# Optimization experiments

Measured on AMD Instinct MI355X. Metric: run time of the kernel, lower is better.

The kernel has to match this reference:

```python
import jax, jax.numpy as jnp
import numpy as np

IN_DIM = 5000
OUT_DIM = 30
K = 50
BATCH = 16384


def setup_inputs() -> dict:
    key = jax.random.key(0)
    ks = jax.random.split(key, 8)
    return {
        "x": jax.random.normal(ks[0], (BATCH, IN_DIM), dtype=jnp.float32),
        "logits": jax.random.normal(ks[1], (IN_DIM,), dtype=jnp.float32),
        "W1": jax.random.normal(ks[2], (IN_DIM, 32), dtype=jnp.float32) * (1.0 / np.sqrt(IN_DIM)),
        "b1": jax.random.normal(ks[3], (32,), dtype=jnp.float32) * 0.01,
        "W2": jax.random.normal(ks[4], (32, 16), dtype=jnp.float32) * (1.0 / np.sqrt(32)),
        "b2": jax.random.normal(ks[5], (16,), dtype=jnp.float32) * 0.01,
        "W3": jax.random.normal(ks[6], (16, OUT_DIM), dtype=jnp.float32) * (1.0 / np.sqrt(16)),
        "b3": jax.random.normal(ks[7], (OUT_DIM,), dtype=jnp.float32) * 0.01,
        "epoch": 10,
        "total_epochs": 100,
    }


def reference(x, logits, W1, b1, W2, b2, W3, b3, epoch, total_epochs):
    # Eval path (training=False): top-k one-hot mask over the learned logits.
    # indices of top-k logits -> k-hot mask of shape [in_dim]
    _, idx = jax.lax.top_k(logits, K)                 # [K]
    mask = jnp.zeros_like(logits).at[idx].set(1.0)    # [in_dim], k-hot
    xm = mask * x                                      # [B, in_dim] gated input
    h = jax.nn.relu(xm @ W1 + b1)                      # [B, 32]
    h = jax.nn.relu(h @ W2 + b2)                       # [B, 16]
    out = h @ W3 + b3                                  # [B, out_dim]
    return out, mask
```

## Files before the change

### kernel.cpp

```cpp
#include <hip/hip_runtime.h>
#include <hip/hip_bf16.h>

#define N_IN 5000
#define K_SEL 50
#define B_ROWS 16384
#define OUT_D 30

__global__ __launch_bounds__(1024) void topk_mask_kernel(
    const float* __restrict__ logits,
    float* __restrict__ mask,
    int* __restrict__ idx_out)
{
    __shared__ unsigned int s_cnt[34];
    __shared__ int s_tick, s_sel;

    const int tid  = threadIdx.x;
    const int lane = tid & 63;

    if (tid < 34) s_cnt[tid] = 0u;
    if (tid == 40) { s_tick = 0; }
    if (tid == 41) { s_sel = 0; }

    unsigned int key[5];
#pragma unroll
    for (int j = 0; j < 5; j++) {
        int i = tid + j * 1024;
        if (i < N_IN) {
            unsigned int b = __float_as_uint(logits[i]);
            key[j] = (b & 0x80000000u) ? ~b : (b | 0x80000000u);
            mask[i] = 0.0f;
        } else {
            key[j] = 0u;
        }
    }
    __syncthreads();

    unsigned int lo = 0u, hi = 0xFFFFFFFFu;
    for (int iter = 0; iter < 32; iter++) {
        if (lo >= hi) break;
        unsigned int mid = lo + ((hi - lo) >> 1) + 1u;
        unsigned int c = 0;
#pragma unroll
        for (int j = 0; j < 5; j++) c += (key[j] >= mid) ? 1u : 0u;
#pragma unroll
        for (int off = 32; off > 0; off >>= 1) c += __shfl_down(c, off, 64);
        if (lane == 0) atomicAdd(&s_cnt[iter], c);
        __syncthreads();
        unsigned int cnt = s_cnt[iter];
        if (cnt >= (unsigned)K_SEL) lo = mid; else hi = mid - 1u;
    }
    const unsigned int KT = lo;

    {
        unsigned int c = 0;
#pragma unroll
        for (int j = 0; j < 5; j++) c += (key[j] > KT) ? 1u : 0u;
#pragma unroll
        for (int off = 32; off > 0; off >>= 1) c += __shfl_down(c, off, 64);
        if (lane == 0) atomicAdd(&s_cnt[33], c);
    }
    __syncthreads();
    const int rem = K_SEL - (int)s_cnt[33];

#pragma unroll
    for (int j = 0; j < 5; j++) {
        int i = tid + j * 1024;
        if (i >= N_IN) continue;
        unsigned int k = key[j];
        bool sel = false;
        if (k > KT) {
            sel = true;
        } else if (k == KT) {
            int t = atomicAdd(&s_tick, 1);
            sel = (t < rem);
        }
        if (sel) {
            int slot = atomicAdd(&s_sel, 1);
            idx_out[slot] = i;
            mask[i] = 1.0f;
        }
    }
}

__global__ __launch_bounds__(256) void gated_mlp_kernel(
    const float* __restrict__ x,
    const float* __restrict__ W1,
    const float* __restrict__ b1,
    const float* __restrict__ W2,
    const float* __restrict__ b2,
    const float* __restrict__ W3,
    const float* __restrict__ b3,
    const int* __restrict__ idx,
    float* __restrict__ out)
{
    __shared__ float xs[64 * 51];
    __shared__ float sW1[K_SEL * 32];
    __shared__ float sW2[32 * 16];
    __shared__ float sW3[16 * OUT_D];
    __shared__ float sb1[32];
    __shared__ float sb2[16];
    __shared__ float sb3[OUT_D];
    __shared__ int   sidx[K_SEL];

    const int tid = threadIdx.x;

    if (tid < K_SEL) sidx[tid] = idx[tid];
    for (int e = tid; e < K_SEL * 32; e += 256) {
        int k = e >> 5, j = e & 31;
        sW1[e] = W1[(size_t)idx[k] * 32 + j];
    }
    for (int e = tid; e < 32 * 16; e += 256) sW2[e] = W2[e];
    for (int e = tid; e < 16 * OUT_D; e += 256) sW3[e] = W3[e];
    if (tid < 32) sb1[tid] = b1[tid];
    if (tid < 16) sb2[tid] = b2[tid];
    if (tid < OUT_D) sb3[tid] = b3[tid];
    __syncthreads();

    const int r  = tid >> 2;
    const int q  = tid & 3;
    const int row = blockIdx.x * 64 + r;
    const float* __restrict__ xrow = x + (size_t)row * N_IN;
    for (int k = q; k < K_SEL; k += 4) {
        xs[r * 51 + k] = xrow[sidx[k]];
    }
    __syncthreads();

    float so_local[OUT_D];
    if (tid < 64) {
        const float* xr = &xs[tid * 51];

        float acc[32];
#pragma unroll
        for (int j = 0; j < 32; j++) acc[j] = sb1[j];
#pragma unroll
        for (int k = 0; k < K_SEL; k++) {
            float xk = xr[k];
#pragma unroll
            for (int j = 0; j < 32; j++) acc[j] = fmaf(xk, sW1[k * 32 + j], acc[j]);
        }

        float h2[16];
#pragma unroll
        for (int j = 0; j < 16; j++) h2[j] = sb2[j];
#pragma unroll
        for (int i = 0; i < 32; i++) {
            float a = fmaxf(acc[i], 0.0f);
#pragma unroll
            for (int j = 0; j < 16; j++) h2[j] = fmaf(a, sW2[i * 16 + j], h2[j]);
        }

#pragma unroll
        for (int j = 0; j < OUT_D; j++) so_local[j] = sb3[j];
#pragma unroll
        for (int i = 0; i < 16; i++) {
            float a = fmaxf(h2[i], 0.0f);
#pragma unroll
            for (int j = 0; j < OUT_D; j++) so_local[j] = fmaf(a, sW3[i * OUT_D + j], so_local[j]);
        }
    }
    __syncthreads();

    float* so = xs;
    if (tid < 64) {
#pragma unroll
        for (int j = 0; j < OUT_D; j++) so[tid * OUT_D + j] = so_local[j];
    }
    __syncthreads();

    float4* out4 = (float4*)(out + (size_t)blockIdx.x * 64 * OUT_D);
    const float4* so4 = (const float4*)so;
    for (int e = tid; e < (64 * OUT_D) / 4; e += 256) {
        out4[e] = so4[e];
    }
}

extern "C" void kernel_launch(void* const* d_in, const int* in_sizes, int n_in,
                              void* d_out, int out_size, void* d_ws, size_t ws_size,
                              hipStream_t stream) {
    const float* x      = (const float*)d_in[0];
    const float* logits = (const float*)d_in[1];
    const float* W1     = (const float*)d_in[2];
    const float* b1     = (const float*)d_in[3];
    const float* W2     = (const float*)d_in[4];
    const float* b2     = (const float*)d_in[5];
    const float* W3     = (const float*)d_in[6];
    const float* b3     = (const float*)d_in[7];

    float* out  = (float*)d_out;
    float* mask = out + (size_t)B_ROWS * OUT_D;
    int*   idx  = (int*)d_ws;

    topk_mask_kernel<<<1, 1024, 0, stream>>>(logits, mask, idx);
    gated_mlp_kernel<<<256, 256, 0, stream>>>(x, W1, b1, W2, b2, W3, b3, idx, out);
}
```

Measured before the change: 432.0 us.

## Spread MLP compute across all block threads and shrink top-k block with early exit

```diff
diff --git a/kernel.cpp b/kernel.cpp
--- a/kernel.cpp
+++ b/kernel.cpp
@@ -6,25 +6,25 @@
 #define B_ROWS 16384
 #define OUT_D 30
 
-__global__ __launch_bounds__(1024) void topk_mask_kernel(
+__global__ __launch_bounds__(256) void topk_mask_kernel(
     const float* __restrict__ logits,
     float* __restrict__ mask,
     int* __restrict__ idx_out)
 {
-    __shared__ unsigned int s_cnt[34];
+    __shared__ unsigned int s_cnt[36];
     __shared__ int s_tick, s_sel;
 
     const int tid  = threadIdx.x;
     const int lane = tid & 63;
 
-    if (tid < 34) s_cnt[tid] = 0u;
-    if (tid == 40) { s_tick = 0; }
-    if (tid == 41) { s_sel = 0; }
-
-    unsigned int key[5];
-#pragma unroll
-    for (int j = 0; j < 5; j++) {
-        int i = tid + j * 1024;
+    if (tid < 36) s_cnt[tid] = 0u;
+    if (tid == 40) s_tick = 0;
+    if (tid == 41) s_sel = 0;
+
+    unsigned int key[20];
+#pragma unroll
+    for (int j = 0; j < 20; j++) {
+        int i = tid + j * 256;
         if (i < N_IN) {
             unsigned int b = __float_as_uint(logits[i]);
             key[j] = (b & 0x80000000u) ? ~b : (b | 0x80000000u);
@@ -36,44 +36,56 @@
     __syncthreads();
 
     unsigned int lo = 0u, hi = 0xFFFFFFFFu;
+    bool exact = false;
+    unsigned int T;
     for (int iter = 0; iter < 32; iter++) {
         if (lo >= hi) break;
         unsigned int mid = lo + ((hi - lo) >> 1) + 1u;
         unsigned int c = 0;
 #pragma unroll
-        for (int j = 0; j < 5; j++) c += (key[j] >= mid) ? 1u : 0u;
+        for (int j = 0; j < 20; j++) c += (key[j] >= mid) ? 1u : 0u;
 #pragma unroll
         for (int off = 32; off > 0; off >>= 1) c += __shfl_down(c, off, 64);
         if (lane == 0) atomicAdd(&s_cnt[iter], c);
         __syncthreads();
         unsigned int cnt = s_cnt[iter];
-        if (cnt >= (unsigned)K_SEL) lo = mid; else hi = mid - 1u;
-    }
+        if (cnt == (unsigned)K_SEL) { T = mid; exact = true; break; }
+        if (cnt > (unsigned)K_SEL) lo = mid; else hi = mid - 1u;
+    }
+
+    if (exact) {
+#pragma unroll
+        for (int j = 0; j < 20; j++) {
+            int i = tid + j * 256;
+            if (i < N_IN && key[j] >= T) {
+                int slot = atomicAdd(&s_sel, 1);
+                idx_out[slot] = i;
+                mask[i] = 1.0f;
+            }
+        }
+        return;
+    }
+
     const unsigned int KT = lo;
-
     {
         unsigned int c = 0;
 #pragma unroll
-        for (int j = 0; j < 5; j++) c += (key[j] > KT) ? 1u : 0u;
+        for (int j = 0; j < 20; j++) c += (key[j] > KT) ? 1u : 0u;
 #pragma unroll
         for (int off = 32; off > 0; off >>= 1) c += __shfl_down(c, off, 64);
-        if (lane == 0) atomicAdd(&s_cnt[33], c);
-    }
-    __syncthreads();
-    const int rem = K_SEL - (int)s_cnt[33];
-
-#pragma unroll
-    for (int j = 0; j < 5; j++) {
-        int i = tid + j * 1024;
+        if (lane == 0) atomicAdd(&s_cnt[35], c);
+    }
+    __syncthreads();
+    const int rem = K_SEL - (int)s_cnt[35];
+
+#pragma unroll
+    for (int j = 0; j < 20; j++) {
+        int i = tid + j * 256;
         if (i >= N_IN) continue;
         unsigned int k = key[j];
         bool sel = false;
-        if (k > KT) {
-            sel = true;
-        } else if (k == KT) {
-            int t = atomicAdd(&s_tick, 1);
-            sel = (t < rem);
-        }
+        if (k > KT) sel = true;
+        else if (k == KT) { int t = atomicAdd(&s_tick, 1); sel = (t < rem); }
         if (sel) {
             int slot = atomicAdd(&s_sel, 1);
             idx_out[slot] = i;
@@ -94,6 +106,8 @@
     float* __restrict__ out)
 {
     __shared__ float xs[64 * 51];
+    __shared__ float h1s[64 * 33];
+    __shared__ float h2s[64 * 17];
     __shared__ float sW1[K_SEL * 32];
     __shared__ float sW2[32 * 16];
     __shared__ float sW3[16 * OUT_D];
@@ -116,61 +130,82 @@
     if (tid < OUT_D) sb3[tid] = b3[tid];
     __syncthreads();
 
-    const int r  = tid >> 2;
-    const int q  = tid & 3;
-    const int row = blockIdx.x * 64 + r;
-    const float* __restrict__ xrow = x + (size_t)row * N_IN;
-    for (int k = q; k < K_SEL; k += 4) {
-        xs[r * 51 + k] = xrow[sidx[k]];
-    }
-    __syncthreads();
-
-    float so_local[OUT_D];
-    if (tid < 64) {
-        const float* xr = &xs[tid * 51];
-
-        float acc[32];
-#pragma unroll
-        for (int j = 0; j < 32; j++) acc[j] = sb1[j];
-#pragma unroll
+    {
+        const int r = tid >> 2;
+        const int q = tid & 3;
+        const int row = blockIdx.x * 64 + r;
+        const float* __restrict__ xrow = x + (size_t)row * N_IN;
+        float g[13];
+#pragma unroll
+        for (int u = 0; u < 13; u++) {
+            int k = q * 13 + u;
+            if (k < K_SEL) g[u] = xrow[sidx[k]];
+        }
+#pragma unroll
+        for (int u = 0; u < 13; u++) {
+            int k = q * 13 + u;
+            if (k < K_SEL) xs[r * 51 + k] = g[u];
+        }
+    }
+    __syncthreads();
+
+    const int r = tid & 63;
+    const int c = tid >> 6;
+
+    {
+        float acc[8];
+#pragma unroll
+        for (int jj = 0; jj < 8; jj++) acc[jj] = sb1[c * 8 + jj];
+        const float* xr = &xs[r * 51];
         for (int k = 0; k < K_SEL; k++) {
             float xk = xr[k];
-#pragma unroll
-            for (int j = 0; j < 32; j++) acc[j] = fmaf(xk, sW1[k * 32 + j], acc[j]);
-        }
-
-        float h2[16];
-#pragma unroll
-        for (int j = 0; j < 16; j++) h2[j] = sb2[j];
+            const float* w = &sW1[k * 32 + c * 8];
+#pragma unroll
+            for (int jj = 0; jj < 8; jj++) acc[jj] = fmaf(xk, w[jj], acc[jj]);
+        }
+#pragma unroll
+        for (int jj = 0; jj < 8; jj++) h1s[r * 33 + c * 8 + jj] = fmaxf(acc[jj], 0.0f);
+    }
+    __syncthreads();
+
+    {
+        float acc[4];
+#pragma unroll
+        for (int jj = 0; jj < 4; jj++) acc[jj] = sb2[c * 4 + jj];
+        const float* hr = &h1s[r * 33];
 #pragma unroll
         for (int i = 0; i < 32; i++) {
-            float a = fmaxf(acc[i], 0.0f);
-#pragma unroll
-            for (int j = 0; j < 16; j++) h2[j] = fmaf(a, sW2[i * 16 + j], h2[j]);
-        }
-
-#pragma unroll
-        for (int j = 0; j < OUT_D; j++) so_local[j] = sb3[j];
+            float a = hr[i];
+            const float* w = &sW2[i * 16 + c * 4];
+#pragma unroll
+            for (int jj = 0; jj < 4; jj++) acc[jj] = fmaf(a, w[jj], acc[jj]);
+        }
+#pragma unroll
+        for (int jj = 0; jj < 4; jj++) h2s[r * 17 + c * 4 + jj] = fmaxf(acc[jj], 0.0f);
+    }
+    __syncthreads();
+
+    {
+        const int j0 = c * 8;
+        const int nj = (c == 3) ? 6 : 8;
+        float acc[8];
+        for (int jj = 0; jj < nj; jj++) acc[jj] = sb3[j0 + jj];
+        const float* hr = &h2s[r * 17];
 #pragma unroll
         for (int i = 0; i < 16; i++) {
-            float a = fmaxf(h2[i], 0.0f);
-#pragma unroll
-            for (int j = 0; j < OUT_D; j++) so_local[j] = fmaf(a, sW3[i * OUT_D + j], so_local[j]);
-        }
-    }
-    __syncthreads();
-
-    float* so = xs;
-    if (tid < 64) {
-#pragma unroll
-        for (int j = 0; j < OUT_D; j++) so[tid * OUT_D + j] = so_local[j];
-    }
-    __syncthreads();
-
-    float4* out4 = (float4*)(out + (size_t)blockIdx.x * 64 * OUT_D);
-    const float4* so4 = (const float4*)so;
-    for (int e = tid; e < (64 * OUT_D) / 4; e += 256) {
-        out4[e] = so4[e];
+            float a = hr[i];
+            const float* w = &sW3[i * OUT_D + j0];
+            for (int jj = 0; jj < nj; jj++) acc[jj] = fmaf(a, w[jj], acc[jj]);
+        }
+        float* so = xs;
+        for (int jj = 0; jj < nj; jj++) so[r * OUT_D + j0 + jj] = acc[jj];
+    }
+    __syncthreads();
+
+    {
+        float4* out4 = (float4*)(out + (size_t)blockIdx.x * 64 * OUT_D);
+        const float4* so4 = (const float4*)xs;
+        for (int e = tid; e < (64 * OUT_D) / 4; e += 256) out4[e] = so4[e];
     }
 }
 
@@ -190,6 +225,6 @@
     float* mask = out + (size_t)B_ROWS * OUT_D;
     int*   idx  = (int*)d_ws;
 
-    topk_mask_kernel<<<1, 1024, 0, stream>>>(logits, mask, idx);
+    topk_mask_kernel<<<1, 256, 0, stream>>>(logits, mask, idx);
     gated_mlp_kernel<<<256, 256, 0, stream>>>(x, W1, b1, W2, b2, W3, b3, idx, out);
 }
```

New measurement: 424.1 us. Within noise of the previous version (-1.8%).
